# Kernel optimization log

Hardware: AMD Instinct MI355X
Metric: run time of the kernel (lower is better)

The kernel has to match this reference:

```python
import jax, jax.numpy as jnp
import numpy as np

B, T, C = 32, 1536, 768
G, Vg = 2, 160  # num_groups, vars_per_group (num_vars=320)
TEMP = 2.0


def setup_inputs() -> dict:
    key = jax.random.key(0)
    kx, kg, kw, kc = jax.random.split(key, 4)
    x = jax.random.normal(kx, (B, T, C), dtype=jnp.float32)
    # Gumbel(0,1) noise, equivalent to torch's -log(Exp(1).sample())
    gumbel = jax.random.gumbel(kg, (B, T, G, Vg), dtype=jnp.float32)
    W_proj = jax.random.normal(kw, (C, G * Vg), dtype=jnp.float32) * (1.0 / np.sqrt(C))
    b_proj = jnp.zeros((G * Vg,), dtype=jnp.float32)
    codebook = jax.random.normal(kc, (G, Vg, C), dtype=jnp.float32)
    return {"x": x, "gumbel": gumbel, "W_proj": W_proj, "b_proj": b_proj, "codebook": codebook}


def reference(x, gumbel, W_proj, b_proj, codebook):
    b, t, c = x.shape
    g, vg, _ = codebook.shape
    logits = (x @ W_proj + b_proj).reshape(b, t, g, vg)          # (B,T,G,Vg)
    probs = jax.nn.softmax((logits + gumbel) / TEMP, axis=-1)    # (B,T,G,Vg)
    codes = jnp.argmax(probs, axis=-1)                           # (B,T,G)
    # Fused codebook contraction: sum over vars AND groups in one GEMM-like einsum,
    # avoiding the naive (B,T,G,Vg,C) broadcast intermediate.
    quantized = jnp.einsum('btgv,gvc->btc', probs, codebook)     # (B,T,C)
    return quantized, codes, probs
```

## Files before the change

### kernel.cpp

```cpp
#include <hip/hip_runtime.h>
#include <hip/hip_bf16.h>
#include <stdint.h>

#define BT_TOK   49152
#define C_DIM    768
#define NVARS    320
#define VG       160
#define NGROUPS  2

__device__ __forceinline__ unsigned short bf16_rne(float f) {
    union { float f; uint32_t u; } v; v.f = f;
    uint32_t u = v.u + 0x7FFFu + ((v.u >> 16) & 1u);
    return (unsigned short)(u >> 16);
}
__device__ __forceinline__ float bf16_to_f(unsigned short h) {
    union { uint32_t u; float f; } v; v.u = ((uint32_t)h) << 16;
    return v.f;
}

typedef __attribute__((ext_vector_type(8))) short bf16x8;
typedef __attribute__((ext_vector_type(4))) float f32x4;

#define GLOBAL_AS __attribute__((address_space(1)))
#define LDS_AS    __attribute__((address_space(3)))
__device__ __forceinline__ void gl2lds16(const void* g, void* l) {
    __builtin_amdgcn_global_load_lds((const GLOBAL_AS void*)g, (LDS_AS void*)l, 16, 0, 0);
}

__global__ __launch_bounds__(256)
void transpose_split(const float* __restrict__ in, unsigned short* __restrict__ hi,
                     unsigned short* __restrict__ lo, int K, int N) {
    int k = blockIdx.x * 256 + threadIdx.x;
    int n = blockIdx.y;
    if (k >= K) return;
    float f = in[(size_t)k * N + n];
    unsigned short h = bf16_rne(f);
    hi[(size_t)n * K + k] = h;
    lo[(size_t)n * K + k] = bf16_rne(f - bf16_to_f(h));
}

template<int BM, int BN, int WM, int WN>
__global__ __launch_bounds__(WM*WN*64, 2)
void gemm1_softmax_fused(const float* __restrict__ X,
                         const unsigned short* __restrict__ Bthi,
                         const unsigned short* __restrict__ Btlo,
                         const float* __restrict__ bias,
                         const float* __restrict__ gumbel,
                         float* __restrict__ probs,
                         float* __restrict__ codes,
                         int M, int N, int K)
{
    constexpr int NW = WM * WN;
    constexpr int ACH    = BM * 4;
    constexpr int nIterB = (BN * 4) / 64;
    constexpr int ABYTES = BM * 32 * 2;
    constexpr int BBYTES = BN * 32 * 2;
    constexpr int BUFBYTES = 2 * ABYTES + 2 * BBYTES;

    extern __shared__ __align__(16) char smem[];

    const int tid  = threadIdx.x;
    const int lane = tid & 63;
    const int wid  = tid >> 6;
    const int wm   = wid % WM;
    const int wn   = wid / WM;
    const int m0   = blockIdx.y * BM;
    const int n0   = blockIdx.x * BN;

    const int r15 = lane & 15;
    const int q   = lane >> 4;

    const int arow  = tid >> 2;
    const int ac    = tid & 3;
    const int aslot = ac ^ ((arow >> 1) & 3);
    const float* aptr = X + (size_t)(m0 + arow) * K + ac * 8;
    const bool adoes = (tid < ACH);

    f32x4 acc[4][4];
#pragma unroll
    for (int i = 0; i < 4; ++i)
#pragma unroll
        for (int j = 0; j < 4; ++j) {
            f32x4 z = {0.f, 0.f, 0.f, 0.f};
            acc[i][j] = z;
        }

    auto issueB = [&](int buf, int k0) {
        char* base = smem + buf * BUFBYTES + 2 * ABYTES;
        for (int i = wid; i < nIterB; i += NW) {
            int slot = i * 64 + lane;
            int row  = slot >> 2, cs = slot & 3;
            int c    = cs ^ ((row >> 1) & 3);
            size_t goff = (size_t)(n0 + row) * K + k0 + c * 8;
            gl2lds16(Bthi + goff, base + i * 1024);
            gl2lds16(Btlo + goff, base + BBYTES + i * 1024);
        }
    };

    float4 av0, av1;
    auto loadA = [&](int k0) {
        if (adoes) {
            av0 = *(const float4*)(aptr + k0);
            av1 = *(const float4*)(aptr + k0 + 4);
        }
    };
    auto writeA = [&](int buf) {
        if (adoes) {
            char* base = smem + buf * BUFBYTES;
            union { unsigned short u[8]; bf16x8 v; } h, l;
            float f[8] = {av0.x, av0.y, av0.z, av0.w, av1.x, av1.y, av1.z, av1.w};
#pragma unroll
            for (int j = 0; j < 8; ++j) {
                h.u[j] = bf16_rne(f[j]);
                l.u[j] = bf16_rne(f[j] - bf16_to_f(h.u[j]));
            }
            *(bf16x8*)(base + arow * 64 + aslot * 16)          = h.v;
            *(bf16x8*)(base + ABYTES + arow * 64 + aslot * 16) = l.v;
        }
    };

    const int NT = K / 32;
    loadA(0);
    issueB(0, 0);
    writeA(0);
    __syncthreads();

    int cur = 0;
    for (int t = 0; t < NT; ++t) {
        if (t + 1 < NT) { loadA((t + 1) * 32); issueB(cur ^ 1, (t + 1) * 32); }

        const unsigned short* sAh = (const unsigned short*)(smem + cur * BUFBYTES);
        const unsigned short* sAl = (const unsigned short*)(smem + cur * BUFBYTES + ABYTES);
        const unsigned short* sBh = (const unsigned short*)(smem + cur * BUFBYTES + 2 * ABYTES);
        const unsigned short* sBl = (const unsigned short*)(smem + cur * BUFBYTES + 2 * ABYTES + BBYTES);

        bf16x8 ah[4], al[4], bh[4], bl[4];
#pragma unroll
        for (int mi = 0; mi < 4; ++mi) {
            int row = wm * 64 + mi * 16 + r15;
            int off = row * 32 + ((q ^ ((row >> 1) & 3)) * 8);
            ah[mi] = *(const bf16x8*)&sAh[off];
            al[mi] = *(const bf16x8*)&sAl[off];
        }
#pragma unroll
        for (int ni = 0; ni < 4; ++ni) {
            int row = wn * 64 + ni * 16 + r15;
            int off = row * 32 + ((q ^ ((row >> 1) & 3)) * 8);
            bh[ni] = *(const bf16x8*)&sBh[off];
            bl[ni] = *(const bf16x8*)&sBl[off];
        }

#pragma unroll
        for (int mi = 0; mi < 4; ++mi)
#pragma unroll
            for (int ni = 0; ni < 4; ++ni) {
                acc[mi][ni] = __builtin_amdgcn_mfma_f32_16x16x32_bf16(ah[mi], bh[ni], acc[mi][ni], 0, 0, 0);
                acc[mi][ni] = __builtin_amdgcn_mfma_f32_16x16x32_bf16(ah[mi], bl[ni], acc[mi][ni], 0, 0, 0);
                acc[mi][ni] = __builtin_amdgcn_mfma_f32_16x16x32_bf16(al[mi], bh[ni], acc[mi][ni], 0, 0, 0);
            }

        if (t + 1 < NT) writeA(cur ^ 1);

        __syncthreads();
        cur ^= 1;
    }

    float* sL = (float*)smem;
    constexpr int LSTR = BN + 1;
#pragma unroll
    for (int ni = 0; ni < 4; ++ni) {
        int col = wn * 64 + ni * 16 + r15;
        float bv = bias[n0 + col];
#pragma unroll
        for (int mi = 0; mi < 4; ++mi) {
            int rbase = wm * 64 + mi * 16 + q * 4;
#pragma unroll
            for (int rr = 0; rr < 4; ++rr)
                sL[(rbase + rr) * LSTR + col] = acc[mi][ni][rr] + bv;
        }
    }
    __syncthreads();

    for (int rg = wid; rg < 2 * BM; rg += NW) {
        const int r = rg >> 1, g = rg & 1;
        const float* gsrc = gumbel + (size_t)(m0 + r) * NVARS + g * VG;
        const float* lrow = sL + r * LSTR + g * VG;
        const bool  has2 = (lane < VG - 128);

        float y0 = (lrow[lane]       + gsrc[lane])       * 0.5f;
        float y1 = (lrow[lane + 64]  + gsrc[lane + 64])  * 0.5f;
        float y2 = has2 ? (lrow[lane + 128] + gsrc[lane + 128]) * 0.5f
                        : -3.402823466e+38f;

        float mx = fmaxf(fmaxf(y0, y1), y2);
#pragma unroll
        for (int off = 32; off > 0; off >>= 1)
            mx = fmaxf(mx, __shfl_xor(mx, off, 64));

        float e0 = expf(y0 - mx);
        float e1 = expf(y1 - mx);
        float e2 = has2 ? expf(y2 - mx) : 0.f;
        float s  = e0 + e1 + e2;
#pragma unroll
        for (int off = 32; off > 0; off >>= 1)
            s += __shfl_xor(s, off, 64);
        const float inv = 1.0f / s;

        float* prow = probs + (size_t)(m0 + r) * NVARS + g * VG;
        prow[lane]      = e0 * inv;
        prow[lane + 64] = e1 * inv;
        if (has2) prow[lane + 128] = e2 * inv;

        float bvv = y0; int bii = lane;
        if (y1 > bvv) { bvv = y1; bii = lane + 64; }
        if (has2 && y2 > bvv) { bvv = y2; bii = lane + 128; }
#pragma unroll
        for (int off = 32; off > 0; off >>= 1) {
            float ov = __shfl_xor(bvv, off, 64);
            int   oi = __shfl_xor(bii, off, 64);
            if (ov > bvv || (ov == bvv && oi < bii)) { bvv = ov; bii = oi; }
        }
        if (lane == 0) codes[(size_t)(m0 + r) * NGROUPS + g] = (float)bii;
    }
}

template<int BM, int BN, int WM, int WN>
__global__ __launch_bounds__(WM*WN*64, (WM*WN+3)/4)
void gemm2_fused(const float* __restrict__ P,
                 const unsigned short* __restrict__ Bthi,
                 const unsigned short* __restrict__ Btlo,
                 float* __restrict__ C,
                 int M, int N, int K)
{
    constexpr int NW = WM * WN;
    constexpr int ACH    = BM * 4;
    constexpr int nIterB = (BN * 4) / 64;
    constexpr int ABYTES = BM * 32 * 2;
    constexpr int BBYTES = BN * 32 * 2;
    constexpr int BUFBYTES = 2 * ABYTES + 2 * BBYTES;

    extern __shared__ __align__(16) char smem[];

    const int tid  = threadIdx.x;
    const int lane = tid & 63;
    const int wid  = tid >> 6;
    const int wm   = wid % WM;
    const int wn   = wid / WM;
    const int m0   = blockIdx.y * BM;
    const int n0   = blockIdx.x * BN;

    const int r15 = lane & 15;
    const int q   = lane >> 4;

    const int arow  = tid >> 2;
    const int ac    = tid & 3;
    const int aslot = ac ^ ((arow >> 1) & 3);
    const float* aptr = P + (size_t)(m0 + arow) * K + ac * 8;
    const bool adoes = (tid < ACH);

    f32x4 acc[4][4];
#pragma unroll
    for (int i = 0; i < 4; ++i)
#pragma unroll
        for (int j = 0; j < 4; ++j) {
            f32x4 z = {0.f, 0.f, 0.f, 0.f};
            acc[i][j] = z;
        }

    auto issueB = [&](int buf, int k0) {
        char* base = smem + buf * BUFBYTES + 2 * ABYTES;
        for (int i = wid; i < nIterB; i += NW) {
            int slot = i * 64 + lane;
            int row  = slot >> 2, cs = slot & 3;
            int c    = cs ^ ((row >> 1) & 3);
            size_t goff = (size_t)(n0 + row) * K + k0 + c * 8;
            gl2lds16(Bthi + goff, base + i * 1024);
            gl2lds16(Btlo + goff, base + BBYTES + i * 1024);
        }
    };

    auto stageA = [&](int buf, int k0) {
        if (adoes) {
            float4 av0 = *(const float4*)(aptr + k0);
            float4 av1 = *(const float4*)(aptr + k0 + 4);
            char* base = smem + buf * BUFBYTES;
            union { unsigned short u[8]; bf16x8 v; } h, l;
            float f[8] = {av0.x, av0.y, av0.z, av0.w, av1.x, av1.y, av1.z, av1.w};
#pragma unroll
            for (int j = 0; j < 8; ++j) {
                h.u[j] = bf16_rne(f[j]);
                l.u[j] = bf16_rne(f[j] - bf16_to_f(h.u[j]));
            }
            *(bf16x8*)(base + arow * 64 + aslot * 16)          = h.v;
            *(bf16x8*)(base + ABYTES + arow * 64 + aslot * 16) = l.v;
        }
    };

    const int NT = K / 32;
    issueB(0, 0);
    stageA(0, 0);
    __syncthreads();

    int cur = 0;
    for (int t = 0; t < NT; ++t) {
        if (t + 1 < NT) { issueB(cur ^ 1, (t + 1) * 32); stageA(cur ^ 1, (t + 1) * 32); }

        const unsigned short* sAh = (const unsigned short*)(smem + cur * BUFBYTES);
        const unsigned short* sAl = (const unsigned short*)(smem + cur * BUFBYTES + ABYTES);
        const unsigned short* sBh = (const unsigned short*)(smem + cur * BUFBYTES + 2 * ABYTES);
        const unsigned short* sBl = (const unsigned short*)(smem + cur * BUFBYTES + 2 * ABYTES + BBYTES);

        bf16x8 ah[4], al[4], bh[4], bl[4];
#pragma unroll
        for (int mi = 0; mi < 4; ++mi) {
            int row = wm * 64 + mi * 16 + r15;
            int off = row * 32 + ((q ^ ((row >> 1) & 3)) * 8);
            ah[mi] = *(const bf16x8*)&sAh[off];
            al[mi] = *(const bf16x8*)&sAl[off];
        }
#pragma unroll
        for (int ni = 0; ni < 4; ++ni) {
            int row = wn * 64 + ni * 16 + r15;
            int off = row * 32 + ((q ^ ((row >> 1) & 3)) * 8);
            bh[ni] = *(const bf16x8*)&sBh[off];
            bl[ni] = *(const bf16x8*)&sBl[off];
        }

#pragma unroll
        for (int mi = 0; mi < 4; ++mi)
#pragma unroll
            for (int ni = 0; ni < 4; ++ni) {
                acc[mi][ni] = __builtin_amdgcn_mfma_f32_16x16x32_bf16(ah[mi], bh[ni], acc[mi][ni], 0, 0, 0);
                acc[mi][ni] = __builtin_amdgcn_mfma_f32_16x16x32_bf16(ah[mi], bl[ni], acc[mi][ni], 0, 0, 0);
                acc[mi][ni] = __builtin_amdgcn_mfma_f32_16x16x32_bf16(al[mi], bh[ni], acc[mi][ni], 0, 0, 0);
            }

        __syncthreads();
        cur ^= 1;
    }

#pragma unroll
    for (int ni = 0; ni < 4; ++ni) {
        int col = n0 + wn * 64 + ni * 16 + r15;
#pragma unroll
        for (int mi = 0; mi < 4; ++mi) {
            int rbase = m0 + wm * 64 + mi * 16 + q * 4;
#pragma unroll
            for (int rr = 0; rr < 4; ++rr)
                C[(size_t)(rbase + rr) * N + col] = acc[mi][ni][rr];
        }
    }
}

__global__ __launch_bounds__(256)
void gumbel_softmax_kernel(float* __restrict__ logits_probs,
                           const float* __restrict__ gumbel,
                           float* __restrict__ codes,
                           unsigned short* __restrict__ phi,
                           unsigned short* __restrict__ plo)
{
    const int wid  = (int)((blockIdx.x * (size_t)blockDim.x + threadIdx.x) >> 6);
    const int lane = threadIdx.x & 63;
    if (wid >= BT_TOK * NGROUPS) return;

    float* base        = logits_probs + (size_t)wid * VG;
    const float* gbase = gumbel       + (size_t)wid * VG;

    const float NEG = -3.402823466e+38f;
    float y[3];
    float mx = NEG;
#pragma unroll
    for (int i = 0; i < 3; ++i) {
        int v = lane + i * 64;
        float val = NEG;
        if (v < VG) val = (base[v] + gbase[v]) * 0.5f;
        y[i] = val;
        mx = fmaxf(mx, val);
    }
#pragma unroll
    for (int off = 32; off > 0; off >>= 1)
        mx = fmaxf(mx, __shfl_xor(mx, off, 64));

    float e[3];
    float s = 0.f;
#pragma unroll
    for (int i = 0; i < 3; ++i) {
        int v = lane + i * 64;
        e[i] = (v < VG) ? expf(y[i] - mx) : 0.f;
        s += e[i];
    }
#pragma unroll
    for (int off = 32; off > 0; off >>= 1)
        s += __shfl_xor(s, off, 64);
    const float inv = 1.0f / s;

#pragma unroll
    for (int i = 0; i < 3; ++i) {
        int v = lane + i * 64;
        if (v < VG) {
            float p = e[i] * inv;
            base[v] = p;
            if (phi) {
                unsigned short h = bf16_rne(p);
                phi[(size_t)wid * VG + v] = h;
                plo[(size_t)wid * VG + v] = bf16_rne(p - bf16_to_f(h));
            }
        }
    }

    float bv = y[0];
    int   bi = lane;
#pragma unroll
    for (int i = 1; i < 3; ++i) {
        int v = lane + i * 64;
        if (v < VG && y[i] > bv) { bv = y[i]; bi = v; }
    }
#pragma unroll
    for (int off = 32; off > 0; off >>= 1) {
        float ov = __shfl_xor(bv, off, 64);
        int   oi = __shfl_xor(bi, off, 64);
        if (ov > bv || (ov == bv && oi < bi)) { bv = ov; bi = oi; }
    }
    if (lane == 0) codes[wid] = (float)bi;
}

__global__ __launch_bounds__(256)
void sgemm64(const float* __restrict__ A, const float* __restrict__ B,
             const float* __restrict__ bias, float* __restrict__ C,
             int M, int N, int K)
{
    const int tid = threadIdx.x;
    const int n0  = blockIdx.x * 64;
    const int m0  = blockIdx.y * 64;

    __shared__ float As[16][64 + 4];
    __shared__ float Bs[16][64];

    const int a_row = tid >> 2;
    const int a_k   = (tid & 3) * 4;
    const int b_row = tid >> 4;
    const int b_col = (tid & 15) * 4;
    const int tx = tid & 15;
    const int ty = tid >> 4;

    float acc[4][4] = {};

    for (int k0 = 0; k0 < K; k0 += 16) {
        float4 av = *(const float4*)(A + (size_t)(m0 + a_row) * K + k0 + a_k);
        float4 bv = *(const float4*)(B + (size_t)(k0 + b_row) * N + n0 + b_col);
        __syncthreads();
        As[a_k + 0][a_row] = av.x;
        As[a_k + 1][a_row] = av.y;
        As[a_k + 2][a_row] = av.z;
        As[a_k + 3][a_row] = av.w;
        *(float4*)&Bs[b_row][b_col] = bv;
        __syncthreads();
#pragma unroll
        for (int k = 0; k < 16; ++k) {
            float4 a4 = *(const float4*)&As[k][ty * 4];
            float4 b4 = *(const float4*)&Bs[k][tx * 4];
            const float a[4] = {a4.x, a4.y, a4.z, a4.w};
            const float b[4] = {b4.x, b4.y, b4.z, b4.w};
#pragma unroll
            for (int r = 0; r < 4; ++r)
#pragma unroll
                for (int c = 0; c < 4; ++c)
                    acc[r][c] = fmaf(a[r], b[c], acc[r][c]);
        }
    }

    float4 bs = make_float4(0.f, 0.f, 0.f, 0.f);
    if (bias) bs = *(const float4*)(bias + n0 + tx * 4);
#pragma unroll
    for (int r = 0; r < 4; ++r) {
        float4 o;
        o.x = acc[r][0] + bs.x;
        o.y = acc[r][1] + bs.y;
        o.z = acc[r][2] + bs.z;
        o.w = acc[r][3] + bs.w;
        *(float4*)(C + (size_t)(m0 + ty * 4 + r) * N + n0 + tx * 4) = o;
    }
}

extern "C" void kernel_launch(void* const* d_in, const int* in_sizes, int n_in,
                              void* d_out, int out_size, void* d_ws, size_t ws_size,
                              hipStream_t stream) {
    const float* x        = (const float*)d_in[0];
    const float* gumbel   = (const float*)d_in[1];
    const float* W_proj   = (const float*)d_in[2];
    const float* b_proj   = (const float*)d_in[3];
    const float* codebook = (const float*)d_in[4];

    float* quantized = (float*)d_out;
    float* codes     = quantized + (size_t)BT_TOK * C_DIM;
    float* probs     = codes + (size_t)BT_TOK * NGROUPS;

    const size_t SZ_W  = (size_t)C_DIM * NVARS * 2;
    const size_t need  = 4 * SZ_W;

    constexpr int SH1 = 2 * (2 * (64 * 32 * 2)  + 2 * (320 * 32 * 2));
    constexpr int SH2 = 2 * (2 * (128 * 32 * 2) + 2 * (384 * 32 * 2));

    if (ws_size >= need) {
        static bool s_init = false;
        if (!s_init) {
            hipFuncSetAttribute(reinterpret_cast<const void*>(&gemm1_softmax_fused<64, 320, 1, 5>),
                                hipFuncAttributeMaxDynamicSharedMemorySize, SH1);
            hipFuncSetAttribute(reinterpret_cast<const void*>(&gemm2_fused<128, 384, 2, 6>),
                                hipFuncAttributeMaxDynamicSharedMemorySize, SH2);
            s_init = true;
        }

        char* ws = (char*)d_ws;
        unsigned short* wthi = (unsigned short*)(ws);
        unsigned short* wtlo = (unsigned short*)(ws + SZ_W);
        unsigned short* cthi = (unsigned short*)(ws + 2 * SZ_W);
        unsigned short* ctlo = (unsigned short*)(ws + 3 * SZ_W);

        transpose_split<<<dim3((C_DIM + 255) / 256, NVARS), 256, 0, stream>>>(
            W_proj, wthi, wtlo, C_DIM, NVARS);
        transpose_split<<<dim3((NVARS + 255) / 256, C_DIM), 256, 0, stream>>>(
            codebook, cthi, ctlo, NVARS, C_DIM);

        gemm1_softmax_fused<64, 320, 1, 5><<<dim3(1, BT_TOK / 64), 320, SH1, stream>>>(
            x, wthi, wtlo, b_proj, gumbel, probs, codes, BT_TOK, NVARS, C_DIM);

        gemm2_fused<128, 384, 2, 6><<<dim3(C_DIM / 384, BT_TOK / 128), 768, SH2, stream>>>(
            probs, cthi, ctlo, quantized, BT_TOK, C_DIM, NVARS);
    } else {
        dim3 g1(NVARS / 64, BT_TOK / 64);
        sgemm64<<<g1, 256, 0, stream>>>(x, W_proj, b_proj, probs, BT_TOK, NVARS, C_DIM);
        gumbel_softmax_kernel<<<BT_TOK * NGROUPS / 4, 256, 0, stream>>>(
            probs, gumbel, codes, nullptr, nullptr);
        dim3 g2(C_DIM / 64, BT_TOK / 64);
        sgemm64<<<g2, 256, 0, stream>>>(probs, codebook, nullptr, quantized, BT_TOK, C_DIM, NVARS);
    }
}
```

Measured before the change: 615.8 us.

## Prefetch A tiles two stages ahead with partial vmcnt barriers and gumbel prefetch

Both split-bf16 GEMM kernels now load the fp32 A tile two K-steps ahead into registers. They replace __syncthreads with a custom barrier that waits with vmcnt(2), so the in-flight A prefetch is not drained at each step. In the second GEMM the A conversion and store move from before the MFMAs to after them. The fused softmax epilogue also prefetches the next row's gumbel noise while processing the current row. This adds register pressure, and correctness depends on the hand-written waitcnt counting and wave ordering.

Measured after the change: 610.9 us. Within noise of the previous version (-0.8%).

```diff
diff --git a/kernel.cpp b/kernel.cpp
--- a/kernel.cpp
+++ b/kernel.cpp
@@ -25,6 +25,14 @@
 #define LDS_AS    __attribute__((address_space(3)))
 __device__ __forceinline__ void gl2lds16(const void* g, void* l) {
     __builtin_amdgcn_global_load_lds((const GLOBAL_AS void*)g, (LDS_AS void*)l, 16, 0, 0);
+}
+
+__device__ __forceinline__ void wg_barrier_leave(bool leave2) {
+    if (leave2) asm volatile("s_waitcnt vmcnt(2) lgkmcnt(0)" ::: "memory");
+    else        asm volatile("s_waitcnt vmcnt(0) lgkmcnt(0)" ::: "memory");
+    __builtin_amdgcn_s_barrier();
+    asm volatile("" ::: "memory");
+    __builtin_amdgcn_sched_barrier(0);
 }
 
 __global__ __launch_bounds__(256)
@@ -52,6 +60,7 @@
 {
     constexpr int NW = WM * WN;
     constexpr int ACH    = BM * 4;
+    constexpr int AW     = ACH / 64;
     constexpr int nIterB = (BN * 4) / 64;
     constexpr int ABYTES = BM * 32 * 2;
     constexpr int BBYTES = BN * 32 * 2;
@@ -75,6 +84,7 @@
     const int aslot = ac ^ ((arow >> 1) & 3);
     const float* aptr = X + (size_t)(m0 + arow) * K + ac * 8;
     const bool adoes = (tid < ACH);
+    const bool awave = (wid < AW);
 
     f32x4 acc[4][4];
 #pragma unroll
@@ -96,19 +106,17 @@
             gl2lds16(Btlo + goff, base + BBYTES + i * 1024);
         }
     };
-
-    float4 av0, av1;
-    auto loadA = [&](int k0) {
+    auto loadA = [&](float4& v0, float4& v1, int k0) {
         if (adoes) {
-            av0 = *(const float4*)(aptr + k0);
-            av1 = *(const float4*)(aptr + k0 + 4);
+            v0 = *(const float4*)(aptr + k0);
+            v1 = *(const float4*)(aptr + k0 + 4);
         }
     };
-    auto writeA = [&](int buf) {
+    auto writeA = [&](int buf, float4 v0, float4 v1) {
         if (adoes) {
             char* base = smem + buf * BUFBYTES;
             union { unsigned short u[8]; bf16x8 v; } h, l;
-            float f[8] = {av0.x, av0.y, av0.z, av0.w, av1.x, av1.y, av1.z, av1.w};
+            float f[8] = {v0.x, v0.y, v0.z, v0.w, v1.x, v1.y, v1.z, v1.w};
 #pragma unroll
             for (int j = 0; j < 8; ++j) {
                 h.u[j] = bf16_rne(f[j]);
@@ -120,14 +128,21 @@
     };
 
     const int NT = K / 32;
-    loadA(0);
+
+    float4 pA0, pA1, nA0, nA1;
+    loadA(pA0, pA1, 0);
     issueB(0, 0);
-    writeA(0);
-    __syncthreads();
+    writeA(0, pA0, pA1);
+    if (NT > 1) loadA(pA0, pA1, 32);
+    wg_barrier_leave(awave && NT > 1);
 
     int cur = 0;
     for (int t = 0; t < NT; ++t) {
-        if (t + 1 < NT) { loadA((t + 1) * 32); issueB(cur ^ 1, (t + 1) * 32); }
+        const bool hasNext  = (t + 1 < NT);
+        const bool hasNext2 = (t + 2 < NT);
+
+        if (hasNext)  issueB(cur ^ 1, (t + 1) * 32);
+        if (hasNext2) loadA(nA0, nA1, (t + 2) * 32);
 
         const unsigned short* sAh = (const unsigned short*)(smem + cur * BUFBYTES);
         const unsigned short* sAl = (const unsigned short*)(smem + cur * BUFBYTES + ABYTES);
@@ -159,9 +174,9 @@
                 acc[mi][ni] = __builtin_amdgcn_mfma_f32_16x16x32_bf16(al[mi], bh[ni], acc[mi][ni], 0, 0, 0);
             }
 
-        if (t + 1 < NT) writeA(cur ^ 1);
-
-        __syncthreads();
+        if (hasNext) { writeA(cur ^ 1, pA0, pA1); pA0 = nA0; pA1 = nA1; }
+
+        wg_barrier_leave(awave && hasNext2);
         cur ^= 1;
     }
 
@@ -181,16 +196,29 @@
     }
     __syncthreads();
 
-    for (int rg = wid; rg < 2 * BM; rg += NW) {
+    const int RGTOT = 2 * BM;
+    const bool has2 = (lane < VG - 128);
+    int rg = wid;
+    float c0 = 0.f, c1 = 0.f, c2 = 0.f;
+    if (rg < RGTOT) {
+        const float* gs = gumbel + (size_t)(m0 + (rg >> 1)) * NVARS + (rg & 1) * VG;
+        c0 = gs[lane]; c1 = gs[lane + 64];
+        c2 = has2 ? gs[lane + 128] : 0.f;
+    }
+    for (; rg < RGTOT; rg += NW) {
+        const int rgn = rg + NW;
+        float n0g = 0.f, n1g = 0.f, n2g = 0.f;
+        if (rgn < RGTOT) {
+            const float* gs = gumbel + (size_t)(m0 + (rgn >> 1)) * NVARS + (rgn & 1) * VG;
+            n0g = gs[lane]; n1g = gs[lane + 64];
+            n2g = has2 ? gs[lane + 128] : 0.f;
+        }
+
         const int r = rg >> 1, g = rg & 1;
-        const float* gsrc = gumbel + (size_t)(m0 + r) * NVARS + g * VG;
         const float* lrow = sL + r * LSTR + g * VG;
-        const bool  has2 = (lane < VG - 128);
-
-        float y0 = (lrow[lane]       + gsrc[lane])       * 0.5f;
-        float y1 = (lrow[lane + 64]  + gsrc[lane + 64])  * 0.5f;
-        float y2 = has2 ? (lrow[lane + 128] + gsrc[lane + 128]) * 0.5f
-                        : -3.402823466e+38f;
+        float y0 = (lrow[lane]       + c0) * 0.5f;
+        float y1 = (lrow[lane + 64]  + c1) * 0.5f;
+        float y2 = has2 ? (lrow[lane + 128] + c2) * 0.5f : -3.402823466e+38f;
 
         float mx = fmaxf(fmaxf(y0, y1), y2);
 #pragma unroll
@@ -221,6 +249,8 @@
             if (ov > bvv || (ov == bvv && oi < bii)) { bvv = ov; bii = oi; }
         }
         if (lane == 0) codes[(size_t)(m0 + r) * NGROUPS + g] = (float)bii;
+
+        c0 = n0g; c1 = n1g; c2 = n2g;
     }
 }
 
@@ -234,6 +264,7 @@
 {
     constexpr int NW = WM * WN;
     constexpr int ACH    = BM * 4;
+    constexpr int AW     = ACH / 64;
     constexpr int nIterB = (BN * 4) / 64;
     constexpr int ABYTES = BM * 32 * 2;
     constexpr int BBYTES = BN * 32 * 2;
@@ -257,6 +288,7 @@
     const int aslot = ac ^ ((arow >> 1) & 3);
     const float* aptr = P + (size_t)(m0 + arow) * K + ac * 8;
     const bool adoes = (tid < ACH);
+    const bool awave = (wid < AW);
 
     f32x4 acc[4][4];
 #pragma unroll
@@ -278,14 +310,17 @@
             gl2lds16(Btlo + goff, base + BBYTES + i * 1024);
         }
     };
-
-    auto stageA = [&](int buf, int k0) {
+    auto loadA = [&](float4& v0, float4& v1, int k0) {
         if (adoes) {
-            float4 av0 = *(const float4*)(aptr + k0);
-            float4 av1 = *(const float4*)(aptr + k0 + 4);
+            v0 = *(const float4*)(aptr + k0);
+            v1 = *(const float4*)(aptr + k0 + 4);
+        }
+    };
+    auto writeA = [&](int buf, float4 v0, float4 v1) {
+        if (adoes) {
             char* base = smem + buf * BUFBYTES;
             union { unsigned short u[8]; bf16x8 v; } h, l;
-            float f[8] = {av0.x, av0.y, av0.z, av0.w, av1.x, av1.y, av1.z, av1.w};
+            float f[8] = {v0.x, v0.y, v0.z, v0.w, v1.x, v1.y, v1.z, v1.w};
 #pragma unroll
             for (int j = 0; j < 8; ++j) {
                 h.u[j] = bf16_rne(f[j]);
@@ -297,13 +332,21 @@
     };
 
     const int NT = K / 32;
+
+    float4 pA0, pA1, nA0, nA1;
+    loadA(pA0, pA1, 0);
     issueB(0, 0);
-    stageA(0, 0);
-    __syncthreads();
+    writeA(0, pA0, pA1);
+    if (NT > 1) loadA(pA0, pA1, 32);
+    wg_barrier_leave(awave && NT > 1);
 
     int cur = 0;
     for (int t = 0; t < NT; ++t) {
-        if (t + 1 < NT) { issueB(cur ^ 1, (t + 1) * 32); stageA(cur ^ 1, (t + 1) * 32); }
+        const bool hasNext  = (t + 1 < NT);
+        const bool hasNext2 = (t + 2 < NT);
+
+        if (hasNext)  issueB(cur ^ 1, (t + 1) * 32);
+        if (hasNext2) loadA(nA0, nA1, (t + 2) * 32);
 
         const unsigned short* sAh = (const unsigned short*)(smem + cur * BUFBYTES);
         const unsigned short* sAl = (const unsigned short*)(smem + cur * BUFBYTES + ABYTES);
@@ -335,7 +378,9 @@
                 acc[mi][ni] = __builtin_amdgcn_mfma_f32_16x16x32_bf16(al[mi], bh[ni], acc[mi][ni], 0, 0, 0);
             }
 
-        __syncthreads();
+        if (hasNext) { writeA(cur ^ 1, pA0, pA1); pA0 = nA0; pA1 = nA1; }
+
+        wg_barrier_leave(awave && hasNext2);
         cur ^= 1;
     }
 
```
